# Performance work log

Hardware: AMD Instinct MI355X
Metric: run time of the kernel (lower is better)

Reference implementation:

```python
import jax, jax.numpy as jnp
import numpy as np

N, E, G = 10000, 160000, 64     # nodes, edges, graphs in batch
T, F_IN, F_OUT, L = 5, 75, 15, 4  # towers, per-tower in (divide_input=False), per-tower out, conv layers
AVG_DEG_LOG = float(np.log(17.0))  # stand-in for PyG histogram stat (source deg=zeros -> NaN)
BN_EPS = 1e-5
STD_EPS = 1e-5


def _u(key, shape):
    fi, fo = shape[-2], shape[-1]
    lim = float(np.sqrt(6.0 / (fi + fo)))
    return jax.random.uniform(key, shape, jnp.float32, -lim, lim)


def setup_inputs():
    key = jax.random.key(0)
    k = iter(jax.random.split(key, 24))
    inp = {}
    inp["x"] = jax.random.randint(next(k), (N, 2), 0, 21)
    inp["edge_index"] = jax.random.randint(next(k), (2, E), 0, N)
    inp["edge_attr"] = jax.random.randint(next(k), (E, 2), 0, 4)
    inp["batch"] = jnp.sort(jax.random.randint(next(k), (N,), 0, G))
    inp["node_emb"] = jax.random.normal(next(k), (21, 75), jnp.float32)
    inp["edge_emb"] = jax.random.normal(next(k), (4, 25), jnp.float32)
    inp["pre_lin_W"] = _u(next(k), (150, 75)); inp["pre_lin_b"] = jnp.zeros((75,), jnp.float32)
    inp["edge_enc_W"] = _u(next(k), (L, 50, F_IN)); inp["edge_enc_b"] = jnp.zeros((L, F_IN), jnp.float32)
    inp["pre_W"] = _u(next(k), (L, T, 3 * F_IN, F_IN)); inp["pre_b"] = jnp.zeros((L, T, F_IN), jnp.float32)
    inp["post_W"] = _u(next(k), (L, T, 13 * F_IN, F_OUT)); inp["post_b"] = jnp.zeros((L, T, F_OUT), jnp.float32)
    inp["lin_W"] = _u(next(k), (L, T * F_OUT, 75)); inp["lin_b"] = jnp.zeros((L, 75), jnp.float32)
    inp["bn_g"] = jnp.ones((L, 75), jnp.float32); inp["bn_b"] = jnp.zeros((L, 75), jnp.float32)
    inp["mlp_W1"] = _u(next(k), (75, 50)); inp["mlp_b1"] = jnp.zeros((50,), jnp.float32)
    inp["mlp_W2"] = _u(next(k), (50, 25)); inp["mlp_b2"] = jnp.zeros((25,), jnp.float32)
    inp["mlp_W3"] = _u(next(k), (25, 1)); inp["mlp_b3"] = jnp.zeros((1,), jnp.float32)
    return inp


def _forward(x, edge_index, edge_attr, batch, node_emb, edge_emb, pre_lin_W, pre_lin_b,
             edge_enc_W, edge_enc_b, pre_W, pre_b, post_W, post_b, lin_W, lin_b,
             bn_g, bn_b, mlp_W1, mlp_b1, mlp_W2, mlp_b2, mlp_W3, mlp_b3):
    # node / edge embeddings -> features
    h = node_emb[x].reshape(N, 150) @ pre_lin_W + pre_lin_b          # [N,75]
    ea = edge_emb[edge_attr].reshape(E, 50)                           # [E,50]
    src, dst = edge_index[0], edge_index[1]  # messages flow src -> dst (x_j=src, x_i=dst)

    cnt = jax.ops.segment_sum(jnp.ones((E,), jnp.float32), dst, num_segments=N)  # in-degree [N]
    deg = jnp.maximum(cnt, 1.0)[:, None, None]
    log_deg = jnp.log(jnp.maximum(cnt, 1.0) + 1.0)[:, None, None]
    amp = log_deg / AVG_DEG_LOG
    att = AVG_DEG_LOG / log_deg
    has = (cnt > 0)[:, None, None]

    for l in range(L):
        e = ea @ edge_enc_W[l] + edge_enc_b[l]                        # [E,75]
        m_in = jnp.concatenate([h[dst], h[src], e], axis=-1)          # [E,225]
        msgs = jnp.einsum('ec,tcf->etf', m_in, pre_W[l]) + pre_b[l]   # [E,T,75]
        s = jax.ops.segment_sum(msgs, dst, num_segments=N)
        mean = s / deg
        mean_sq = jax.ops.segment_sum(msgs * msgs, dst, num_segments=N) / deg
        std = jnp.sqrt(jax.nn.relu(mean_sq - mean * mean) + STD_EPS)
        mn = jnp.where(has, jax.ops.segment_min(msgs, dst, num_segments=N), 0.0)
        mx = jnp.where(has, jax.ops.segment_max(msgs, dst, num_segments=N), 0.0)
        agg = jnp.concatenate([mean, mn, mx, std], axis=-1)           # [N,T,300]
        scaled = jnp.concatenate([agg, agg * amp, agg * att], axis=-1)  # [N,T,900]
        out = jnp.concatenate([jnp.broadcast_to(h[:, None, :], (N, T, F_IN)), scaled], axis=-1)  # [N,T,975]
        post = jnp.einsum('ntc,tcf->ntf', out, post_W[l]) + post_b[l]  # [N,T,15]
        hc = post.reshape(N, T * F_OUT) @ lin_W[l] + lin_b[l]          # [N,75]
        mu = hc.mean(axis=0)
        var = hc.var(axis=0)  # biased, matches BatchNorm1d training mode
        h = jax.nn.relu((hc - mu) / jnp.sqrt(var + BN_EPS) * bn_g[l] + bn_b[l])

    g = jax.ops.segment_sum(h, batch, num_segments=G)                 # global_add_pool [G,75]
    g = jax.nn.relu(g @ mlp_W1 + mlp_b1)
    g = jax.nn.relu(g @ mlp_W2 + mlp_b2)
    return g @ mlp_W3 + mlp_b3                                        # [G,1]


def reference(x, edge_index, edge_attr, batch, node_emb, edge_emb, pre_lin_W, pre_lin_b,
              edge_enc_W, edge_enc_b, pre_W, pre_b, post_W, post_b, lin_W, lin_b,
              bn_g, bn_b, mlp_W1, mlp_b1, mlp_W2, mlp_b2, mlp_W3, mlp_b3):
    return _forward(x, edge_index, edge_attr, batch, node_emb, edge_emb, pre_lin_W, pre_lin_b,
                    edge_enc_W, edge_enc_b, pre_W, pre_b, post_W, post_b, lin_W, lin_b,
                    bn_g, bn_b, mlp_W1, mlp_b1, mlp_W2, mlp_b2, mlp_W3, mlp_b3)
```

## Files before the change

kernel.cpp:

```cpp
#include <hip/hip_runtime.h>
#include <math.h>

#define NN 10000
#define NE 160000
#define NG 64
#define NT 5
#define NL 4
#define ADL 2.833213344056216f

#define OFF_H      0
#define OFF_HC     750000
#define OFF_P      1500000
#define OFF_Q      5250000
#define OFF_AGG    9000000
#define OFF_RLUT   24000000
#define OFF_INVDEG 24006000
#define OFF_AMP    24016000
#define OFF_ATT    24026000
#define OFF_STATS  24036000
#define OFF_GPOOL  24036160
#define OFF_INT    24118960

__global__ void k_zero_cnt(int* cnt){
    int i = blockIdx.x*256 + threadIdx.x;
    if (i < NN) cnt[i] = 0;
}

__global__ __launch_bounds__(256) void k_h0(const int* __restrict__ x,
        const float* __restrict__ node_emb, const float* __restrict__ plW,
        const float* __restrict__ plb, float* __restrict__ h){
    __shared__ float s_emb[21*75];
    __shared__ float s_W[150*75];
    __shared__ float s_b[75];
    int tid = threadIdx.x;
    for (int i = tid; i < 21*75; i += 256) s_emb[i] = node_emb[i];
    for (int i = tid; i < 150*75; i += 256) s_W[i] = plW[i];
    if (tid < 75) s_b[tid] = plb[tid];
    __syncthreads();
    for (int out = blockIdx.x*256 + tid; out < NN*75; out += gridDim.x*256){
        int n = out / 75, f = out - n*75;
        int x0 = x[2*n], x1 = x[2*n+1];
        float acc = s_b[f];
        const float* e0 = s_emb + x0*75;
        const float* e1 = s_emb + x1*75;
        #pragma unroll 5
        for (int k = 0; k < 75; k++)
            acc += e0[k]*s_W[k*75+f] + e1[k]*s_W[(75+k)*75+f];
        h[out] = acc;
    }
}

__global__ void k_hist(const int* __restrict__ ei, int* __restrict__ cnt){
    int e = blockIdx.x*256 + threadIdx.x;
    if (e < NE) atomicAdd(&cnt[ei[NE + e]], 1);
}

__global__ void k_scan(const int* __restrict__ cnt, int* __restrict__ eoff){
    __shared__ int buf[256];
    __shared__ int carry;
    int tid = threadIdx.x;
    if (tid == 0){ carry = 0; eoff[0] = 0; }
    __syncthreads();
    for (int base = 0; base < NN; base += 256){
        int v = (base + tid < NN) ? cnt[base + tid] : 0;
        buf[tid] = v; __syncthreads();
        for (int off = 1; off < 256; off <<= 1){
            int t2 = (tid >= off) ? buf[tid - off] : 0;
            __syncthreads();
            buf[tid] += t2;
            __syncthreads();
        }
        int inc = buf[tid] + carry;
        if (base + tid < NN) eoff[base + tid + 1] = inc;
        __syncthreads();
        if (tid == 255) carry = inc;
        __syncthreads();
    }
}

__global__ void k_nodestats(const int* __restrict__ cnt, const int* __restrict__ eoff,
        float* __restrict__ invdeg, float* __restrict__ amp, float* __restrict__ att,
        int* __restrict__ cursor){
    int n = blockIdx.x*256 + threadIdx.x;
    if (n >= NN) return;
    int c = cnt[n];
    cursor[n] = eoff[n];
    float cf = (float)c;
    float dg = cf < 1.f ? 1.f : cf;
    invdeg[n] = 1.f / dg;
    float ld = logf(dg + 1.f);
    amp[n] = ld / ADL;
    att[n] = ADL / ld;
}

__global__ void k_scatter(const int* __restrict__ ei, const int* __restrict__ ea,
        int* __restrict__ cursor, int* __restrict__ esrc, int* __restrict__ ecombo){
    int e = blockIdx.x*256 + threadIdx.x;
    if (e >= NE) return;
    int src = ei[e], dst = ei[NE + e];
    int pos = atomicAdd(&cursor[dst], 1);
    esrc[pos] = src;
    ecombo[pos] = ea[2*e]*4 + ea[2*e+1];
}

__global__ __launch_bounds__(384) void k_pq(const float* __restrict__ h,
        const float* __restrict__ preW, const float* __restrict__ preb,
        const float* __restrict__ edge_emb, const float* __restrict__ encW,
        const float* __restrict__ encb, int l,
        float* __restrict__ P, float* __restrict__ Q,
        float* __restrict__ Rlut, float* __restrict__ stats){
    __shared__ float smem[10675];
    int tid = threadIdx.x;
    int bx = blockIdx.x;

    if (bx == 318){
        for (int i = tid; i < 150; i += 384) stats[i] = 0.f;
        return;
    }
    if (bx >= 313){
        int t = bx - 313;
        float* s_encW = smem;
        float* s_ev   = smem + 3750;
        float* s_wc   = smem + 4950;
        float* s_ee   = smem + 10575;
        for (int i = tid; i < 3750; i += 384) s_encW[i] = encW[(size_t)l*3750 + i];
        for (int i = tid; i < 100; i += 384) s_ee[i] = edge_emb[i];
        const float* wcsrc = preW + (((size_t)(l*NT + t))*225 + 150)*75;
        for (int i = tid; i < 5625; i += 384) s_wc[i] = wcsrc[i];
        __syncthreads();
        for (int task = tid; task < 1200; task += 384){
            int b = task/75, m = task - 75*b;
            int a0 = b >> 2, a1 = b & 3;
            float s = encb[l*75 + m];
            for (int k = 0; k < 25; k++)
                s += s_ee[a0*25+k]*s_encW[k*75+m] + s_ee[a1*25+k]*s_encW[(25+k)*75+m];
            s_ev[task] = s;
        }
        __syncthreads();
        for (int task = tid; task < 1200; task += 384){
            int b = task/75, f = task - 75*b;
            float r = preb[((size_t)l*NT + t)*75 + f];
            const float* ev = s_ev + b*75;
            #pragma unroll 5
            for (int m = 0; m < 75; m++) r += ev[m]*s_wc[m*75 + f];
            Rlut[b*375 + t*75 + f] = r;
        }
        return;
    }

    float* h_t = smem;
    int base = bx*32;
    for (int idx = tid; idx < 32*75; idx += 384){
        int i = idx/75, m = idx - 75*i;
        int n = base + i;
        h_t[i*76 + m] = (n < NN) ? h[(size_t)n*75 + m] : 0.f;
    }
    __syncthreads();
    int j = tid;
    if (j >= 375) return;
    int t = j/75, f = j - 75*t;
    const float* wbase = preW + ((size_t)(l*NT + t))*225*75 + f;
    float accP[32], accQ[32];
    #pragma unroll
    for (int i = 0; i < 32; i++){ accP[i] = 0.f; accQ[i] = 0.f; }
    for (int m = 0; m < 72; m += 4){
        float wa0 = wbase[(m+0)*75], wa1 = wbase[(m+1)*75];
        float wa2 = wbase[(m+2)*75], wa3 = wbase[(m+3)*75];
        float wb0 = wbase[(75+m+0)*75], wb1 = wbase[(75+m+1)*75];
        float wb2 = wbase[(75+m+2)*75], wb3 = wbase[(75+m+3)*75];
        #pragma unroll
        for (int i = 0; i < 32; i++){
            const float4 hv = *(const float4*)&h_t[i*76 + m];
            accP[i] += hv.x*wa0 + hv.y*wa1 + hv.z*wa2 + hv.w*wa3;
            accQ[i] += hv.x*wb0 + hv.y*wb1 + hv.z*wb2 + hv.w*wb3;
        }
    }
    for (int m = 72; m < 75; m++){
        float wa = wbase[m*75], wb = wbase[(75+m)*75];
        #pragma unroll
        for (int i = 0; i < 32; i++){
            float v = h_t[i*76 + m];
            accP[i] += v*wa; accQ[i] += v*wb;
        }
    }
    for (int i = 0; i < 32; i++){
        int n = base + i;
        if (n < NN){ P[(size_t)n*375 + j] = accP[i]; Q[(size_t)n*375 + j] = accQ[i]; }
    }
}

#define JS 47
__global__ __launch_bounds__(64) void k_agg(const float* __restrict__ P,
        const float* __restrict__ Q, const float* __restrict__ Rlut,
        const int* __restrict__ eoff, const int* __restrict__ esrc,
        const int* __restrict__ ecombo, const float* __restrict__ invdeg,
        float* __restrict__ agg){
    int n = blockIdx.y;
    int j = blockIdx.x*JS + threadIdx.x;
    if (threadIdx.x >= JS || j >= 375) return;
    int lo = eoff[n], hi = eoff[n+1];
    float p = P[(size_t)n*375 + j];
    float sum = 0.f, sq = 0.f, mn = 3.4e38f, mx = -3.4e38f;
    int e = lo;
    for (; e + 4 <= hi; e += 4){
        int s0 = esrc[e],   s1 = esrc[e+1],   s2 = esrc[e+2],   s3 = esrc[e+3];
        int c0 = ecombo[e], c1 = ecombo[e+1], c2 = ecombo[e+2], c3 = ecombo[e+3];
        float q0 = Q[(size_t)s0*375 + j];
        float q1 = Q[(size_t)s1*375 + j];
        float q2 = Q[(size_t)s2*375 + j];
        float q3 = Q[(size_t)s3*375 + j];
        float r0 = Rlut[c0*375 + j];
        float r1 = Rlut[c1*375 + j];
        float r2 = Rlut[c2*375 + j];
        float r3 = Rlut[c3*375 + j];
        float m0 = p + q0 + r0, m1 = p + q1 + r1;
        float m2 = p + q2 + r2, m3 = p + q3 + r3;
        sum += m0 + m1 + m2 + m3;
        sq  += m0*m0 + m1*m1 + m2*m2 + m3*m3;
        mn = fminf(mn, fminf(fminf(m0, m1), fminf(m2, m3)));
        mx = fmaxf(mx, fmaxf(fmaxf(m0, m1), fmaxf(m2, m3)));
    }
    for (; e < hi; e++){
        int s = esrc[e], cm = ecombo[e];
        float m = p + Q[(size_t)s*375 + j] + Rlut[cm*375 + j];
        sum += m; sq += m*m;
        mn = fminf(mn, m); mx = fmaxf(mx, m);
    }
    float id = invdeg[n];
    bool has = hi > lo;
    float mean = sum*id;
    float msq  = sq*id;
    float var = msq - mean*mean; var = var > 0.f ? var : 0.f;
    float sd = sqrtf(var + 1e-5f);
    float mnv = has ? mn : 0.f;
    float mxv = has ? mx : 0.f;
    int t = j/75, f = j - 75*t;
    float* a = agg + ((size_t)n*NT + t)*300;
    a[f] = mean; a[75+f] = mnv; a[150+f] = mxv; a[225+f] = sd;
}

#define TK 25
#define PADA 27
#define NB 128
__global__ __launch_bounds__(256, 8) void k_post(const float* __restrict__ h,
        const float* __restrict__ agg, const float* __restrict__ postW,
        const float* __restrict__ postb, const float* __restrict__ amp,
        const float* __restrict__ att, int l, float* __restrict__ postbase){
    __shared__ float s_a[NB*PADA];
    __shared__ float s_w[3][TK*16];
    int t = blockIdx.y;
    int z = blockIdx.z;
    int nbase = blockIdx.x*NB;
    int tid = threadIdx.x;
    int fg  = (tid & 3)*4;
    int sub = tid >> 2;
    const float* Wt = postW + ((size_t)(l*NT + t))*975*15;
    float a1[2][4], a2[2][4], a3[2][4];
    #pragma unroll
    for (int j = 0; j < 2; j++)
        #pragma unroll
        for (int f = 0; f < 4; f++){ a1[j][f]=0.f; a2[j][f]=0.f; a3[j][f]=0.f; }

    if (z == 0){
        for (int kt = 0; kt < 75; kt += TK){
            for (int idx = tid; idx < NB*TK; idx += 256){
                int row = idx / TK, c = idx - row*TK;
                int n = nbase + row;
                s_a[row*PADA + c] = (n < NN) ? h[(size_t)n*75 + kt + c] : 0.f;
            }
            for (int idx = tid; idx < TK*16; idx += 256){
                int c = idx >> 4, f = idx & 15;
                s_w[0][idx] = (f < 15) ? Wt[(kt + c)*15 + f] : 0.f;
            }
            __syncthreads();
            for (int k = 0; k < TK; k++){
                const float4 w1 = *(const float4*)&s_w[0][k*16 + fg];
                #pragma unroll
                for (int j = 0; j < 2; j++){
                    float v = s_a[(sub + 64*j)*PADA + k];
                    a1[j][0] += v*w1.x; a1[j][1] += v*w1.y;
                    a1[j][2] += v*w1.z; a1[j][3] += v*w1.w;
                }
            }
            __syncthreads();
        }
        const float* pb = postb + (l*NT + t)*15;
        #pragma unroll
        for (int j = 0; j < 2; j++){
            int n = nbase + sub + 64*j;
            if (n >= NN) continue;
            float* dst = postbase + (size_t)n*75 + t*15;
            #pragma unroll
            for (int f = 0; f < 4; f++)
                if (fg + f < 15) dst[fg + f] = a1[j][f] + pb[fg + f];
        }
        return;
    }

    int kbeg = (z-1)*50, kend = kbeg + 50;
    for (int kt = kbeg; kt < kend; kt += TK){
        for (int idx = tid; idx < NB*TK; idx += 256){
            int row = idx / TK, c = idx - row*TK;
            int n = nbase + row;
            s_a[row*PADA + c] = (n < NN) ? agg[(size_t)n*1500 + t*300 + kt + c] : 0.f;
        }
        for (int idx = tid; idx < TK*16; idx += 256){
            int c = idx >> 4, f = idx & 15;
            float v1 = 0.f, v2 = 0.f, v3 = 0.f;
            if (f < 15){
                v1 = Wt[( 75 + kt + c)*15 + f];
                v2 = Wt[(375 + kt + c)*15 + f];
                v3 = Wt[(675 + kt + c)*15 + f];
            }
            s_w[0][idx] = v1; s_w[1][idx] = v2; s_w[2][idx] = v3;
        }
        __syncthreads();
        for (int k = 0; k < TK; k++){
            const float4 w1 = *(const float4*)&s_w[0][k*16 + fg];
            const float4 w2 = *(const float4*)&s_w[1][k*16 + fg];
            const float4 w3 = *(const float4*)&s_w[2][k*16 + fg];
            #pragma unroll
            for (int j = 0; j < 2; j++){
                float v = s_a[(sub + 64*j)*PADA + k];
                a1[j][0] += v*w1.x; a1[j][1] += v*w1.y;
                a1[j][2] += v*w1.z; a1[j][3] += v*w1.w;
                a2[j][0] += v*w2.x; a2[j][1] += v*w2.y;
                a2[j][2] += v*w2.z; a2[j][3] += v*w2.w;
                a3[j][0] += v*w3.x; a3[j][1] += v*w3.y;
                a3[j][2] += v*w3.z; a3[j][3] += v*w3.w;
            }
        }
        __syncthreads();
    }

    float* postv = postbase + (size_t)z*750000;
    #pragma unroll
    for (int j = 0; j < 2; j++){
        int n = nbase + sub + 64*j;
        if (n >= NN) continue;
        float am = amp[n], at = att[n];
        float* dst = postv + (size_t)n*75 + t*15;
        #pragma unroll
        for (int f = 0; f < 4; f++)
            if (fg + f < 15)
                dst[fg + f] = a1[j][f] + am*a2[j][f] + at*a3[j][f];
    }
}

__global__ __launch_bounds__(256) void k_lin(const float* __restrict__ postbase,
        const float* __restrict__ linW, const float* __restrict__ linb,
        int l, float* __restrict__ hc, float* __restrict__ stats){
    __shared__ float p_l[32*75];
    __shared__ float w_l[75*75];
    __shared__ float hc_l[32*75];
    int tid = threadIdx.x;
    int base = blockIdx.x*32;
    for (int i = tid; i < 75*75; i += 256) w_l[i] = linW[(size_t)l*5625 + i];
    for (int i = tid; i < 32*75; i += 256){
        int n = base + i/75;
        size_t idx = (size_t)base*75 + i;
        float v = 0.f;
        if (n < NN){
            #pragma unroll
            for (int z = 0; z < 7; z++) v += postbase[idx + (size_t)z*750000];
        }
        p_l[i] = v;
    }
    __syncthreads();
    for (int task = tid; task < 2400; task += 256){
        int i = task/75, o = task - 75*i;
        float s = linb[l*75 + o];
        const float* pl = p_l + i*75;
        #pragma unroll 5
        for (int j = 0; j < 75; j++) s += pl[j]*w_l[j*75 + o];
        hc_l[task] = s;
        if (base + i < NN) hc[(size_t)(base+i)*75 + o] = s;
    }
    __syncthreads();
    if (tid < 75){
        int nv = NN - base; if (nv > 32) nv = 32;
        float s1 = 0.f, s2 = 0.f;
        for (int i = 0; i < nv; i++){
            float v = hc_l[i*75 + tid];
            s1 += v; s2 += v*v;
        }
        atomicAdd(&stats[tid], s1);
        atomicAdd(&stats[75+tid], s2);
    }
}

__global__ void k_bnapply(const float* __restrict__ hc, const float* __restrict__ stats,
        const float* __restrict__ bng, const float* __restrict__ bnb, int l,
        float* __restrict__ h){
    int idx = blockIdx.x*256 + threadIdx.x;
    if (idx >= NN*75) return;
    int col = idx % 75;
    float mu = stats[col]*(1.0f/NN);
    float var = stats[75+col]*(1.0f/NN) - mu*mu;
    float inv = rsqrtf(var + 1e-5f);
    float v = (hc[idx] - mu)*inv*bng[l*75+col] + bnb[l*75+col];
    h[idx] = v > 0.f ? v : 0.f;
}

__global__ __launch_bounds__(256) void k_pool(const float* __restrict__ h,
        const int* __restrict__ batch, float* __restrict__ gpool){
    int g = blockIdx.x, tid = threadIdx.x;
    int lo = 0, hi = NN;
    while (lo < hi){ int mid = (lo+hi)>>1; if (batch[mid] < g) lo = mid+1; else hi = mid; }
    int start = lo;
    lo = start; hi = NN;
    while (lo < hi){ int mid = (lo+hi)>>1; if (batch[mid] < g+1) lo = mid+1; else hi = mid; }
    int end = lo;
    __shared__ float red[225];
    if (tid < 225){
        int col = tid % 75, rep = tid / 75;
        float acc = 0.f;
        for (int i = start + rep; i < end; i += 3) acc += h[(size_t)i*75 + col];
        red[tid] = acc;
    }
    __syncthreads();
    if (tid < 75) gpool[g*75 + tid] = red[tid] + red[75+tid] + red[150+tid];
}

__global__ __launch_bounds__(256) void k_mlp(const float* __restrict__ gpool,
        const float* __restrict__ W1, const float* __restrict__ b1,
        const float* __restrict__ W2, const float* __restrict__ b2,
        const float* __restrict__ W3, const float* __restrict__ b3,
        float* __restrict__ out){
    __shared__ float w1[75*50];
    __shared__ float w2[50*25];
    __shared__ float gp[8*75];
    __shared__ float t1[8*50];
    __shared__ float t2[8*25];
    int tid = threadIdx.x;
    int gbase = blockIdx.x*8;
    for (int i = tid; i < 75*50; i += 256) w1[i] = W1[i];
    for (int i = tid; i < 50*25; i += 256) w2[i] = W2[i];
    for (int i = tid; i < 8*75; i += 256) gp[i] = gpool[gbase*75 + i];
    __syncthreads();
    for (int task = tid; task < 8*50; task += 256){
        int g = task/50, j = task - 50*g;
        float s = b1[j];
        const float* gv = gp + g*75;
        #pragma unroll 5
        for (int k = 0; k < 75; k++) s += gv[k]*w1[k*50+j];
        t1[task] = s > 0.f ? s : 0.f;
    }
    __syncthreads();
    for (int task = tid; task < 8*25; task += 256){
        int g = task/25, j = task - 25*g;
        float s = b2[j];
        const float* tv = t1 + g*50;
        #pragma unroll 5
        for (int k = 0; k < 50; k++) s += tv[k]*w2[k*25+j];
        t2[task] = s > 0.f ? s : 0.f;
    }
    __syncthreads();
    if (tid < 8){
        float s = b3[0];
        const float* tv = t2 + tid*25;
        #pragma unroll
        for (int k = 0; k < 25; k++) s += tv[k]*W3[k];
        out[gbase + tid] = s;
    }
}

extern "C" void kernel_launch(void* const* d_in, const int* in_sizes, int n_in,
                              void* d_out, int out_size, void* d_ws, size_t ws_size,
                              hipStream_t stream){
    const int* x          = (const int*)d_in[0];
    const int* edge_index = (const int*)d_in[1];
    const int* edge_attr  = (const int*)d_in[2];
    const int* batch      = (const int*)d_in[3];
    const float* node_emb = (const float*)d_in[4];
    const float* edge_emb = (const float*)d_in[5];
    const float* pre_lin_W= (const float*)d_in[6];
    const float* pre_lin_b= (const float*)d_in[7];
    const float* encW     = (const float*)d_in[8];
    const float* encb     = (const float*)d_in[9];
    const float* preW     = (const float*)d_in[10];
    const float* preb     = (const float*)d_in[11];
    const float* postW    = (const float*)d_in[12];
    const float* postb    = (const float*)d_in[13];
    const float* linW     = (const float*)d_in[14];
    const float* linb     = (const float*)d_in[15];
    const float* bng      = (const float*)d_in[16];
    const float* bnb      = (const float*)d_in[17];
    const float* mlpW1    = (const float*)d_in[18];
    const float* mlpb1    = (const float*)d_in[19];
    const float* mlpW2    = (const float*)d_in[20];
    const float* mlpb2    = (const float*)d_in[21];
    const float* mlpW3    = (const float*)d_in[22];
    const float* mlpb3    = (const float*)d_in[23];

    float* ws = (float*)d_ws;
    float* h      = ws + OFF_H;
    float* hc     = ws + OFF_HC;
    float* P      = ws + OFF_P;
    float* Q      = ws + OFF_Q;
    float* agg    = ws + OFF_AGG;
    float* Rlut   = ws + OFF_RLUT;
    float* invdeg = ws + OFF_INVDEG;
    float* amp    = ws + OFF_AMP;
    float* att    = ws + OFF_ATT;
    float* stats  = ws + OFF_STATS;
    float* gpool  = ws + OFF_GPOOL;
    float* postbase = ws + OFF_P;
    int* iw     = (int*)(ws + OFF_INT);
    int* cnt    = iw;
    int* eoff   = cnt + NN;
    int* cursor = eoff + NN + 2;
    int* esrc   = cursor + NN;
    int* ecombo = esrc + NE;

    k_zero_cnt<<<40, 256, 0, stream>>>(cnt);
    k_h0<<<640, 256, 0, stream>>>(x, node_emb, pre_lin_W, pre_lin_b, h);
    k_hist<<<625, 256, 0, stream>>>(edge_index, cnt);
    k_scan<<<1, 256, 0, stream>>>(cnt, eoff);
    k_nodestats<<<40, 256, 0, stream>>>(cnt, eoff, invdeg, amp, att, cursor);
    k_scatter<<<625, 256, 0, stream>>>(edge_index, edge_attr, cursor, esrc, ecombo);

    for (int l = 0; l < NL; l++){
        k_pq<<<319, 384, 0, stream>>>(h, preW, preb, edge_emb, encW, encb, l,
                                      P, Q, Rlut, stats);
        k_agg<<<dim3(8, NN), 64, 0, stream>>>(P, Q, Rlut, eoff, esrc, ecombo, invdeg, agg);
        k_post<<<dim3(80, 5, 7), 256, 0, stream>>>(h, agg, postW, postb, amp, att, l, postbase);
        k_lin<<<313, 256, 0, stream>>>(postbase, linW, linb, l, hc, stats);
        k_bnapply<<<2930, 256, 0, stream>>>(hc, stats, bng, bnb, l, h);
    }

    k_pool<<<NG, 256, 0, stream>>>(h, batch, gpool);
    k_mlp<<<8, 256, 0, stream>>>(gpool, mlpW1, mlpb1, mlpW2, mlpb2, mlpW3, mlpb3, (float*)d_out);
}
```

Before: 979.1 us.

## Loop towers inside k_post and stage outputs in LDS for coalesced stores

k_post now handles all five towers inside each block, over 64 nodes instead of 128. Each tower's partial results are staged in a shared-memory tile and then written to postbase with contiguous float4 stores, replacing the scattered 15-float strided writes. The postbase slice stride is padded so the last partial block can write whole rows, and k_lin reads with the new stride. The trade-off is fewer blocks, one node per thread (less reuse of weights loaded from shared memory), extra LDS use and lower occupancy bounds.

```diff
diff --git a/kernel.cpp b/kernel.cpp
--- a/kernel.cpp
+++ b/kernel.cpp
@@ -240,111 +240,97 @@
 }
 
 #define TK 25
-#define PADA 27
-#define NB 128
-__global__ __launch_bounds__(256, 8) void k_post(const float* __restrict__ h,
+#define SAS 27
+#define NBP 64
+#define PSTRIDE 753600
+__global__ __launch_bounds__(256, 5) void k_post(const float* __restrict__ h,
         const float* __restrict__ agg, const float* __restrict__ postW,
         const float* __restrict__ postb, const float* __restrict__ amp,
         const float* __restrict__ att, int l, float* __restrict__ postbase){
-    __shared__ float s_a[NB*PADA];
+    __shared__ float s_a[NBP*SAS];
     __shared__ float s_w[3][TK*16];
-    int t = blockIdx.y;
-    int z = blockIdx.z;
-    int nbase = blockIdx.x*NB;
+    __shared__ float post_l[NBP*75];
+    int z = blockIdx.y;
+    int nbase = blockIdx.x*NBP;
     int tid = threadIdx.x;
     int fg  = (tid & 3)*4;
     int sub = tid >> 2;
-    const float* Wt = postW + ((size_t)(l*NT + t))*975*15;
-    float a1[2][4], a2[2][4], a3[2][4];
-    #pragma unroll
-    for (int j = 0; j < 2; j++)
-        #pragma unroll
-        for (int f = 0; f < 4; f++){ a1[j][f]=0.f; a2[j][f]=0.f; a3[j][f]=0.f; }
-
-    if (z == 0){
-        for (int kt = 0; kt < 75; kt += TK){
-            for (int idx = tid; idx < NB*TK; idx += 256){
-                int row = idx / TK, c = idx - row*TK;
-                int n = nbase + row;
-                s_a[row*PADA + c] = (n < NN) ? h[(size_t)n*75 + kt + c] : 0.f;
+    int n = nbase + sub;
+    float am = 0.f, at = 0.f;
+    if (z && n < NN){ am = amp[n]; at = att[n]; }
+
+    for (int t = 0; t < NT; t++){
+        const float* Wt = postW + ((size_t)(l*NT + t))*975*15;
+        float a1[4] = {0,0,0,0}, a2[4] = {0,0,0,0}, a3[4] = {0,0,0,0};
+        if (z == 0){
+            for (int kt = 0; kt < 75; kt += TK){
+                for (int idx = tid; idx < NBP*TK; idx += 256){
+                    int row = idx/TK, c = idx - row*TK;
+                    int nn = nbase + row;
+                    s_a[row*SAS + c] = (nn < NN) ? h[(size_t)nn*75 + kt + c] : 0.f;
+                }
+                for (int idx = tid; idx < TK*16; idx += 256){
+                    int c = idx >> 4, f = idx & 15;
+                    s_w[0][idx] = (f < 15) ? Wt[(kt + c)*15 + f] : 0.f;
+                }
+                __syncthreads();
+                for (int k = 0; k < TK; k++){
+                    float v = s_a[sub*SAS + k];
+                    const float4 w1 = *(const float4*)&s_w[0][k*16 + fg];
+                    a1[0] += v*w1.x; a1[1] += v*w1.y;
+                    a1[2] += v*w1.z; a1[3] += v*w1.w;
+                }
+                __syncthreads();
             }
-            for (int idx = tid; idx < TK*16; idx += 256){
-                int c = idx >> 4, f = idx & 15;
-                s_w[0][idx] = (f < 15) ? Wt[(kt + c)*15 + f] : 0.f;
-            }
-            __syncthreads();
-            for (int k = 0; k < TK; k++){
-                const float4 w1 = *(const float4*)&s_w[0][k*16 + fg];
-                #pragma unroll
-                for (int j = 0; j < 2; j++){
-                    float v = s_a[(sub + 64*j)*PADA + k];
-                    a1[j][0] += v*w1.x; a1[j][1] += v*w1.y;
-                    a1[j][2] += v*w1.z; a1[j][3] += v*w1.w;
-                }
-            }
-            __syncthreads();
-        }
-        const float* pb = postb + (l*NT + t)*15;
-        #pragma unroll
-        for (int j = 0; j < 2; j++){
-            int n = nbase + sub + 64*j;
-            if (n >= NN) continue;
-            float* dst = postbase + (size_t)n*75 + t*15;
+            const float* pb = postb + (l*NT + t)*15;
             #pragma unroll
             for (int f = 0; f < 4; f++)
-                if (fg + f < 15) dst[fg + f] = a1[j][f] + pb[fg + f];
-        }
-        return;
-    }
-
-    int kbeg = (z-1)*50, kend = kbeg + 50;
-    for (int kt = kbeg; kt < kend; kt += TK){
-        for (int idx = tid; idx < NB*TK; idx += 256){
-            int row = idx / TK, c = idx - row*TK;
-            int n = nbase + row;
-            s_a[row*PADA + c] = (n < NN) ? agg[(size_t)n*1500 + t*300 + kt + c] : 0.f;
-        }
-        for (int idx = tid; idx < TK*16; idx += 256){
-            int c = idx >> 4, f = idx & 15;
-            float v1 = 0.f, v2 = 0.f, v3 = 0.f;
-            if (f < 15){
-                v1 = Wt[( 75 + kt + c)*15 + f];
-                v2 = Wt[(375 + kt + c)*15 + f];
-                v3 = Wt[(675 + kt + c)*15 + f];
+                if (fg + f < 15)
+                    post_l[sub*75 + t*15 + fg + f] = a1[f] + pb[fg + f];
+        } else {
+            int kbeg = (z-1)*50;
+            for (int kt = kbeg; kt < kbeg + 50; kt += TK){
+                for (int idx = tid; idx < NBP*TK; idx += 256){
+                    int row = idx/TK, c = idx - row*TK;
+                    int nn = nbase + row;
+                    s_a[row*SAS + c] = (nn < NN) ? agg[(size_t)nn*1500 + t*300 + kt + c] : 0.f;
+                }
+                for (int idx = tid; idx < TK*16; idx += 256){
+                    int c = idx >> 4, f = idx & 15;
+                    float v1 = 0.f, v2 = 0.f, v3 = 0.f;
+                    if (f < 15){
+                        v1 = Wt[( 75 + kt + c)*15 + f];
+                        v2 = Wt[(375 + kt + c)*15 + f];
+                        v3 = Wt[(675 + kt + c)*15 + f];
+                    }
+                    s_w[0][idx] = v1; s_w[1][idx] = v2; s_w[2][idx] = v3;
+                }
+                __syncthreads();
+                for (int k = 0; k < TK; k++){
+                    float v = s_a[sub*SAS + k];
+                    const float4 w1 = *(const float4*)&s_w[0][k*16 + fg];
+                    const float4 w2 = *(const float4*)&s_w[1][k*16 + fg];
+                    const float4 w3 = *(const float4*)&s_w[2][k*16 + fg];
+                    a1[0] += v*w1.x; a1[1] += v*w1.y;
+                    a1[2] += v*w1.z; a1[3] += v*w1.w;
+                    a2[0] += v*w2.x; a2[1] += v*w2.y;
+                    a2[2] += v*w2.z; a2[3] += v*w2.w;
+                    a3[0] += v*w3.x; a3[1] += v*w3.y;
+                    a3[2] += v*w3.z; a3[3] += v*w3.w;
+                }
+                __syncthreads();
             }
-            s_w[0][idx] = v1; s_w[1][idx] = v2; s_w[2][idx] = v3;
-        }
-        __syncthreads();
-        for (int k = 0; k < TK; k++){
-            const float4 w1 = *(const float4*)&s_w[0][k*16 + fg];
-            const float4 w2 = *(const float4*)&s_w[1][k*16 + fg];
-            const float4 w3 = *(const float4*)&s_w[2][k*16 + fg];
             #pragma unroll
-            for (int j = 0; j < 2; j++){
-                float v = s_a[(sub + 64*j)*PADA + k];
-                a1[j][0] += v*w1.x; a1[j][1] += v*w1.y;
-                a1[j][2] += v*w1.z; a1[j][3] += v*w1.w;
-                a2[j][0] += v*w2.x; a2[j][1] += v*w2.y;
-                a2[j][2] += v*w2.z; a2[j][3] += v*w2.w;
-                a3[j][0] += v*w3.x; a3[j][1] += v*w3.y;
-                a3[j][2] += v*w3.z; a3[j][3] += v*w3.w;
-            }
-        }
-        __syncthreads();
-    }
-
-    float* postv = postbase + (size_t)z*750000;
-    #pragma unroll
-    for (int j = 0; j < 2; j++){
-        int n = nbase + sub + 64*j;
-        if (n >= NN) continue;
-        float am = amp[n], at = att[n];
-        float* dst = postv + (size_t)n*75 + t*15;
-        #pragma unroll
-        for (int f = 0; f < 4; f++)
-            if (fg + f < 15)
-                dst[fg + f] = a1[j][f] + am*a2[j][f] + at*a3[j][f];
-    }
+            for (int f = 0; f < 4; f++)
+                if (fg + f < 15)
+                    post_l[sub*75 + t*15 + fg + f] = a1[f] + am*a2[f] + at*a3[f];
+        }
+    }
+    __syncthreads();
+    float4* dst4 = (float4*)(postbase + (size_t)z*PSTRIDE + (size_t)nbase*75);
+    const float4* src4 = (const float4*)post_l;
+    for (int i = tid; i < NBP*75/4; i += 256)
+        dst4[i] = src4[i];
 }
 
 __global__ __launch_bounds__(256) void k_lin(const float* __restrict__ postbase,
@@ -362,7 +348,7 @@
         float v = 0.f;
         if (n < NN){
             #pragma unroll
-            for (int z = 0; z < 7; z++) v += postbase[idx + (size_t)z*750000];
+            for (int z = 0; z < 7; z++) v += postbase[idx + (size_t)z*PSTRIDE];
         }
         p_l[i] = v;
     }
@@ -524,7 +510,7 @@
         k_pq<<<319, 384, 0, stream>>>(h, preW, preb, edge_emb, encW, encb, l,
                                       P, Q, Rlut, stats);
         k_agg<<<dim3(8, NN), 64, 0, stream>>>(P, Q, Rlut, eoff, esrc, ecombo, invdeg, agg);
-        k_post<<<dim3(80, 5, 7), 256, 0, stream>>>(h, agg, postW, postb, amp, att, l, postbase);
+        k_post<<<dim3(157, 7), 256, 0, stream>>>(h, agg, postW, postb, amp, att, l, postbase);
         k_lin<<<313, 256, 0, stream>>>(postbase, linW, linb, l, hc, stats);
         k_bnapply<<<2930, 256, 0, stream>>>(hc, stats, bng, bnb, l, h);
     }
```

After: 1.727 ms. 1.76x slower.
